# Optimization experiments

Hardware: AMD Instinct MI355X
Metric: run time of the kernel (lower is better)

Reference implementation:

```python
import jax, jax.numpy as jnp
import numpy as np

B, N_IN, N_HID, N_OUT = 4096, 1024, 4096, 1024

def setup_inputs() -> dict:
    key = jax.random.key(0)
    k_x, k_w1, k_b1, k_w2, k_b2 = jax.random.split(key, 5)
    # Per-node LiveNet weights, batched: each hidden neuron = relu(sum_i w_i * in_i + b),
    # each output neuron = linear sum over hidden neurons.
    s1 = 1.0 / np.sqrt(N_IN)
    s2 = 1.0 / np.sqrt(N_HID)
    return {
        "x": jax.random.normal(k_x, (B, N_IN), dtype=jnp.float32),
        "W1": jax.random.uniform(k_w1, (N_IN, N_HID), jnp.float32, -s1, s1),
        "b1": jax.random.uniform(k_b1, (N_HID,), jnp.float32, -s1, s1),
        "W2": jax.random.uniform(k_w2, (N_HID, N_OUT), jnp.float32, -s2, s2),
        "b2": jax.random.uniform(k_b2, (N_OUT,), jnp.float32, -s2, s2),
    }

def reference(x, W1, b1, W2, b2):
    # Batched equivalent of LiveNet's per-node traversal:
    # inputs[i].set_output(x[:, i:i+1]); each hidden neuron computes
    # relu(weighted sum of parents + bias); each output node is a linear
    # weighted sum of hidden outputs; outputs concatenated along dim=1.
    h = jax.nn.relu(x @ W1 + b1)          # [B, N_HID]
    y = h @ W2 + b2                        # [B, N_OUT]
    return y
```

## Files before the change

kernel.cpp:

```cpp
#include <hip/hip_runtime.h>
#include <stdint.h>

#define BDIM  4096
#define NIN   1024
#define NHID  4096
#define NOUT  1024

typedef unsigned short u16;
typedef unsigned int   u32;
typedef __attribute__((ext_vector_type(8))) __bf16 bf16x8;
typedef __attribute__((ext_vector_type(4))) float  f32x4;

__device__ __forceinline__ u16 f32_to_bf16_rne(float f) {
    u32 u = __builtin_bit_cast(u32, f);
    u = (u + 0x7fffu + ((u >> 16) & 1u)) >> 16;
    return (u16)u;
}

__device__ __forceinline__ void transpose_tile(
    const float* __restrict__ in, u16* __restrict__ out,
    int R, int C, int bx, int by, float (*tile)[33]) {
    const int rt = by * 32, ct = bx * 32;
    const int tid = threadIdx.x;
    const int c  = tid & 31;
    const int r4 = tid >> 5;
#pragma unroll
    for (int rr = 0; rr < 4; ++rr) {
        int r = r4 * 4 + rr;
        tile[r][c] = in[(size_t)(rt + r) * C + (ct + c)];
    }
    __syncthreads();
#pragma unroll
    for (int rr = 0; rr < 4; ++rr) {
        int r = r4 * 4 + rr;
        out[(size_t)(ct + r) * R + (rt + c)] = f32_to_bf16_rne(tile[c][r]);
    }
}

__global__ void prepass(const float* __restrict__ x,  u16* __restrict__ x_bf,
                        const float* __restrict__ W1, u16* __restrict__ W1t,
                        const float* __restrict__ W2, u16* __restrict__ W2t) {
    __shared__ float tile[32][33];
    const int b = blockIdx.x;
    if (b < 4096) {
        int i = b * 256 + threadIdx.x;
        float4 v = ((const float4*)x)[i];
        ushort4 o;
        o.x = f32_to_bf16_rne(v.x); o.y = f32_to_bf16_rne(v.y);
        o.z = f32_to_bf16_rne(v.z); o.w = f32_to_bf16_rne(v.w);
        ((ushort4*)x_bf)[i] = o;
    } else if (b < 8192) {
        int t = b - 4096;
        transpose_tile(W1, W1t, NIN, NHID, t & 127, t >> 7, tile);
    } else {
        int t = b - 8192;
        transpose_tile(W2, W2t, NHID, NOUT, t & 31, t >> 5, tile);
    }
}

__global__ __launch_bounds__(256) void gemm_bt_relu(
    const u16* __restrict__ A, const u16* __restrict__ Bt,
    const float* __restrict__ bias, u16* __restrict__ outp,
    int M, int N, int K)
{
    constexpr int MI = 4, NI = 4;
    __shared__ __align__(16) u16 smemA[128 * 64];
    __shared__ __align__(16) u16 smemB[128 * 64];

    const int tid  = threadIdx.x;
    const int lane = tid & 63;
    const int wave = tid >> 6;
    const int rowBase = blockIdx.y * 128;
    const int colBase = blockIdx.x * 128;
    const int wrow = (wave >> 1) * 64;
    const int wcol = (wave & 1) * 64;

    f32x4 acc[MI][NI] = {};

    const int srow    = lane >> 3;
    const int chunkSw = (lane & 7) ^ srow;
    const int gcol    = chunkSw * 8;
    const int fr = lane & 15;
    const int fq = lane >> 4;
    const int sw = fr & 7;

    for (int k0 = 0; k0 < K; k0 += 64) {
        __syncthreads();
#pragma unroll
        for (int t = 0; t < 4; ++t) {
            int region = wave * 4 + t;
            int arow = rowBase + region * 8 + srow;
            const u16* g = A + (size_t)arow * K + k0 + gcol;
            __builtin_amdgcn_global_load_lds(
                (const __attribute__((address_space(1))) u32*)g,
                (__attribute__((address_space(3))) u32*)(smemA + region * 512),
                16, 0, 0);
        }
#pragma unroll
        for (int t = 0; t < 4; ++t) {
            int region = wave * 4 + t;
            int brow = colBase + region * 8 + srow;
            const u16* g = Bt + (size_t)brow * K + k0 + gcol;
            __builtin_amdgcn_global_load_lds(
                (const __attribute__((address_space(1))) u32*)g,
                (__attribute__((address_space(3))) u32*)(smemB + region * 512),
                16, 0, 0);
        }
        __builtin_amdgcn_s_waitcnt(0);
        __syncthreads();

#pragma unroll
        for (int s = 0; s < 2; ++s) {
            const int co = ((s * 4 + fq) ^ sw) * 16;
            const char* aB = (const char*)smemA + (wrow + fr) * 128 + co;
            const char* bB = (const char*)smemB + (wcol + fr) * 128 + co;
            bf16x8 af[MI], bfv[NI];
#pragma unroll
            for (int mi = 0; mi < MI; ++mi)
                af[mi] = *(const bf16x8*)(aB + mi * 2048);
#pragma unroll
            for (int ni = 0; ni < NI; ++ni)
                bfv[ni] = *(const bf16x8*)(bB + ni * 2048);
#pragma unroll
            for (int mi = 0; mi < MI; ++mi)
#pragma unroll
                for (int ni = 0; ni < NI; ++ni)
                    acc[mi][ni] = __builtin_amdgcn_mfma_f32_16x16x32_bf16(
                        af[mi], bfv[ni], acc[mi][ni], 0, 0, 0);
        }
    }

    const int col0 = colBase + wcol + fr;
    const int row0 = rowBase + wrow + (fq << 2);
#pragma unroll
    for (int ni = 0; ni < NI; ++ni) {
        const int col = col0 + ni * 16;
        const float bv = bias[col];
#pragma unroll
        for (int mi = 0; mi < MI; ++mi) {
            const int row = row0 + mi * 16;
#pragma unroll
            for (int r = 0; r < 4; ++r) {
                float v = acc[mi][ni][r] + bv;
                v = v > 0.f ? v : 0.f;
                outp[(size_t)(row + r) * N + col] = f32_to_bf16_rne(v);
            }
        }
    }
}

__global__ __launch_bounds__(256) void gemm2_splitk(
    const u16* __restrict__ A, const u16* __restrict__ Bt,
    float* __restrict__ out0, float* __restrict__ pextra,
    int M, int N, int K, int Kchunk)
{
    constexpr int MI = 4, NI = 4;
    __shared__ __align__(16) u16 smemA[128 * 64];
    __shared__ __align__(16) u16 smemB[128 * 64];

    const int tid  = threadIdx.x;
    const int lane = tid & 63;
    const int wave = tid >> 6;
    const int rowBase = blockIdx.y * 128;
    const int colBase = blockIdx.x * 128;
    const int z    = blockIdx.z;
    const int kBeg = z * Kchunk;
    const int kEnd = kBeg + Kchunk;
    const int wrow = (wave >> 1) * 64;
    const int wcol = (wave & 1) * 64;

    f32x4 acc[MI][NI] = {};

    const int srow    = lane >> 3;
    const int chunkSw = (lane & 7) ^ srow;
    const int gcol    = chunkSw * 8;
    const int fr = lane & 15;
    const int fq = lane >> 4;
    const int sw = fr & 7;

    for (int k0 = kBeg; k0 < kEnd; k0 += 64) {
        __syncthreads();
#pragma unroll
        for (int t = 0; t < 4; ++t) {
            int region = wave * 4 + t;
            int arow = rowBase + region * 8 + srow;
            const u16* g = A + (size_t)arow * K + k0 + gcol;
            __builtin_amdgcn_global_load_lds(
                (const __attribute__((address_space(1))) u32*)g,
                (__attribute__((address_space(3))) u32*)(smemA + region * 512),
                16, 0, 0);
        }
#pragma unroll
        for (int t = 0; t < 4; ++t) {
            int region = wave * 4 + t;
            int brow = colBase + region * 8 + srow;
            const u16* g = Bt + (size_t)brow * K + k0 + gcol;
            __builtin_amdgcn_global_load_lds(
                (const __attribute__((address_space(1))) u32*)g,
                (__attribute__((address_space(3))) u32*)(smemB + region * 512),
                16, 0, 0);
        }
        __builtin_amdgcn_s_waitcnt(0);
        __syncthreads();

#pragma unroll
        for (int s = 0; s < 2; ++s) {
            const int co = ((s * 4 + fq) ^ sw) * 16;
            const char* aB = (const char*)smemA + (wrow + fr) * 128 + co;
            const char* bB = (const char*)smemB + (wcol + fr) * 128 + co;
            bf16x8 af[MI], bfv[NI];
#pragma unroll
            for (int mi = 0; mi < MI; ++mi)
                af[mi] = *(const bf16x8*)(aB + mi * 2048);
#pragma unroll
            for (int ni = 0; ni < NI; ++ni)
                bfv[ni] = *(const bf16x8*)(bB + ni * 2048);
#pragma unroll
            for (int mi = 0; mi < MI; ++mi)
#pragma unroll
                for (int ni = 0; ni < NI; ++ni)
                    acc[mi][ni] = __builtin_amdgcn_mfma_f32_16x16x32_bf16(
                        af[mi], bfv[ni], acc[mi][ni], 0, 0, 0);
        }
    }

    float* outp = (z == 0) ? out0 : (pextra + (size_t)(z - 1) * M * N);
    const int col0 = colBase + wcol + fr;
    const int row0 = rowBase + wrow + (fq << 2);
#pragma unroll
    for (int ni = 0; ni < NI; ++ni) {
        const int col = col0 + ni * 16;
#pragma unroll
        for (int mi = 0; mi < MI; ++mi) {
            const int row = row0 + mi * 16;
#pragma unroll
            for (int r = 0; r < 4; ++r)
                outp[(size_t)(row + r) * N + col] = acc[mi][ni][r];
        }
    }
}

__global__ void splitk_reduce(float* __restrict__ out0,
                              const float* __restrict__ pextra,
                              const float* __restrict__ bias,
                              int n4, int nCols4) {
    int i = blockIdx.x * blockDim.x + threadIdx.x;
    if (i >= n4) return;
    float4 v = ((const float4*)out0)[i];
    const size_t s4 = (size_t)n4;
#pragma unroll
    for (int s = 0; s < 3; ++s) {
        float4 p = ((const float4*)pextra)[i + s * s4];
        v.x += p.x; v.y += p.y; v.z += p.z; v.w += p.w;
    }
    float4 bv = ((const float4*)bias)[i & (nCols4 - 1)];
    v.x += bv.x; v.y += bv.y; v.z += bv.z; v.w += bv.w;
    ((float4*)out0)[i] = v;
}

extern "C" void kernel_launch(void* const* d_in, const int* in_sizes, int n_in,
                              void* d_out, int out_size, void* d_ws, size_t ws_size,
                              hipStream_t stream) {
    const float* x  = (const float*)d_in[0];
    const float* W1 = (const float*)d_in[1];
    const float* b1 = (const float*)d_in[2];
    const float* W2 = (const float*)d_in[3];
    const float* b2 = (const float*)d_in[4];

    char* ws = (char*)d_ws;
    const size_t MB = 1024 * 1024;
    u16*   W2t  = (u16*)(ws + 0 * MB);
    u16*   h_bf = (u16*)(ws + 8 * MB);
    u16*   x_bf = (u16*)(ws + 40 * MB);
    u16*   W1t  = (u16*)(ws + 48 * MB);
    float* pex  = (float*)(ws + 56 * MB);

    prepass<<<12288, 256, 0, stream>>>(x, x_bf, W1, W1t, W2, W2t);

    gemm_bt_relu<<<dim3(NHID / 128, BDIM / 128), 256, 0, stream>>>(
        x_bf, W1t, b1, h_bf, BDIM, NHID, NIN);

    gemm2_splitk<<<dim3(NOUT / 128, BDIM / 128, 4), 256, 0, stream>>>(
        h_bf, W2t, (float*)d_out, pex, BDIM, NOUT, NHID, NHID / 4);

    int rn4 = BDIM * NOUT / 4;
    splitk_reduce<<<(rn4 + 255) / 256, 256, 0, stream>>>(
        (float*)d_out, pex, b2, rn4, NOUT / 4);
}
```

Measured before the change: 210.1 us.

## Replace split-K reduce kernel with atomic accumulation and vectorize weight transpose

The second GEMM now splits K in two instead of four and accumulates partial results directly into a zeroed output with atomicAdd. The first split adds the bias, which removes the partial-sum workspace and the separate reduce kernel. The weight transpose in the prepass now uses float4 loads and 8-element bf16 stores. Costs added: a memset of the output, scattered per-element atomics, fewer blocks for the second GEMM, and only half the threads active in the transpose store phase.

```diff
diff --git a/kernel.cpp b/kernel.cpp
--- a/kernel.cpp
+++ b/kernel.cpp
@@ -22,18 +22,26 @@
     int R, int C, int bx, int by, float (*tile)[33]) {
     const int rt = by * 32, ct = bx * 32;
     const int tid = threadIdx.x;
-    const int c  = tid & 31;
-    const int r4 = tid >> 5;
-#pragma unroll
-    for (int rr = 0; rr < 4; ++rr) {
-        int r = r4 * 4 + rr;
-        tile[r][c] = in[(size_t)(rt + r) * C + (ct + c)];
+    {
+        const int r  = tid >> 3;
+        const int c4 = (tid & 7) * 4;
+        float4 v = *(const float4*)(in + (size_t)(rt + r) * C + ct + c4);
+        tile[r][c4 + 0] = v.x; tile[r][c4 + 1] = v.y;
+        tile[r][c4 + 2] = v.z; tile[r][c4 + 3] = v.w;
     }
     __syncthreads();
-#pragma unroll
-    for (int rr = 0; rr < 4; ++rr) {
-        int r = r4 * 4 + rr;
-        out[(size_t)(ct + r) * R + (rt + c)] = f32_to_bf16_rne(tile[c][r]);
+    if (tid < 128) {
+        const int oc = tid >> 2;
+        const int ch = tid & 3;
+        u16 tmp[8];
+#pragma unroll
+        for (int j = 0; j < 8; ++j)
+            tmp[j] = f32_to_bf16_rne(tile[ch * 8 + j][oc]);
+        u16* dst = out + (size_t)(ct + oc) * R + rt + ch * 8;
+        ushort4 lo = {tmp[0], tmp[1], tmp[2], tmp[3]};
+        ushort4 hi = {tmp[4], tmp[5], tmp[6], tmp[7]};
+        *(ushort4*)dst = lo;
+        *(ushort4*)(dst + 4) = hi;
     }
 }
 
@@ -151,7 +159,7 @@
 
 __global__ __launch_bounds__(256) void gemm2_splitk(
     const u16* __restrict__ A, const u16* __restrict__ Bt,
-    float* __restrict__ out0, float* __restrict__ pextra,
+    const float* __restrict__ bias, float* __restrict__ out0,
     int M, int N, int K, int Kchunk)
 {
     constexpr int MI = 4, NI = 4;
@@ -224,38 +232,21 @@
         }
     }
 
-    float* outp = (z == 0) ? out0 : (pextra + (size_t)(z - 1) * M * N);
     const int col0 = colBase + wcol + fr;
     const int row0 = rowBase + wrow + (fq << 2);
 #pragma unroll
     for (int ni = 0; ni < NI; ++ni) {
         const int col = col0 + ni * 16;
+        const float bv = (z == 0) ? bias[col] : 0.f;
 #pragma unroll
         for (int mi = 0; mi < MI; ++mi) {
             const int row = row0 + mi * 16;
 #pragma unroll
             for (int r = 0; r < 4; ++r)
-                outp[(size_t)(row + r) * N + col] = acc[mi][ni][r];
-        }
-    }
-}
-
-__global__ void splitk_reduce(float* __restrict__ out0,
-                              const float* __restrict__ pextra,
-                              const float* __restrict__ bias,
-                              int n4, int nCols4) {
-    int i = blockIdx.x * blockDim.x + threadIdx.x;
-    if (i >= n4) return;
-    float4 v = ((const float4*)out0)[i];
-    const size_t s4 = (size_t)n4;
-#pragma unroll
-    for (int s = 0; s < 3; ++s) {
-        float4 p = ((const float4*)pextra)[i + s * s4];
-        v.x += p.x; v.y += p.y; v.z += p.z; v.w += p.w;
-    }
-    float4 bv = ((const float4*)bias)[i & (nCols4 - 1)];
-    v.x += bv.x; v.y += bv.y; v.z += bv.z; v.w += bv.w;
-    ((float4*)out0)[i] = v;
+                atomicAdd(&out0[(size_t)(row + r) * N + col],
+                          acc[mi][ni][r] + bv);
+        }
+    }
 }
 
 extern "C" void kernel_launch(void* const* d_in, const int* in_sizes, int n_in,
@@ -269,21 +260,18 @@
 
     char* ws = (char*)d_ws;
     const size_t MB = 1024 * 1024;
-    u16*   W2t  = (u16*)(ws + 0 * MB);
-    u16*   h_bf = (u16*)(ws + 8 * MB);
-    u16*   x_bf = (u16*)(ws + 40 * MB);
-    u16*   W1t  = (u16*)(ws + 48 * MB);
-    float* pex  = (float*)(ws + 56 * MB);
+    u16* W2t  = (u16*)(ws + 0 * MB);
+    u16* h_bf = (u16*)(ws + 8 * MB);
+    u16* x_bf = (u16*)(ws + 40 * MB);
+    u16* W1t  = (u16*)(ws + 48 * MB);
+
+    hipMemsetAsync(d_out, 0, (size_t)BDIM * NOUT * sizeof(float), stream);
 
     prepass<<<12288, 256, 0, stream>>>(x, x_bf, W1, W1t, W2, W2t);
 
     gemm_bt_relu<<<dim3(NHID / 128, BDIM / 128), 256, 0, stream>>>(
         x_bf, W1t, b1, h_bf, BDIM, NHID, NIN);
 
-    gemm2_splitk<<<dim3(NOUT / 128, BDIM / 128, 4), 256, 0, stream>>>(
-        h_bf, W2t, (float*)d_out, pex, BDIM, NOUT, NHID, NHID / 4);
-
-    int rn4 = BDIM * NOUT / 4;
-    splitk_reduce<<<(rn4 + 255) / 256, 256, 0, stream>>>(
-        (float*)d_out, pex, b2, rn4, NOUT / 4);
-}
+    gemm2_splitk<<<dim3(NOUT / 128, BDIM / 128, 2), 256, 0, stream>>>(
+        h_bf, W2t, b2, (float*)d_out, BDIM, NOUT, NHID, NHID / 2);
+}
```

Measured after the change: 209.4 us. About the same (-0.3%).
